# Kernel tuning notes

Hardware: AMD Instinct MI355X
Metric: run time of the kernel (lower is better)

Reference implementation:

```python
import jax, jax.numpy as jnp
import numpy as np

# LSNNParameters defaults (norse)
TAU_SYN_INV = 200.0     # 1/tau_syn
TAU_MEM_INV = 100.0     # 1/tau_mem
TAU_ADAPT_INV = 1.0 / 800.0  # 1/tau_adapt
V_LEAK = 0.0
V_TH = 1.0
V_RESET = 0.0
BETA = 1.8
DT = 0.001

B, IN_F, OUT_F = 8192, 512, 1024


def setup_inputs() -> dict:
    key = jax.random.key(0)
    k0, k1, k2, k3, k4, k5, k6 = jax.random.split(key, 7)
    input_spikes = (jax.random.uniform(k0, (B, IN_F)) < 0.2).astype(jnp.float32)
    z = (jax.random.uniform(k1, (B, OUT_F)) < 0.2).astype(jnp.float32)
    v = jax.random.normal(k2, (B, OUT_F)) * 0.5
    i = jax.random.normal(k3, (B, OUT_F)) * 0.5
    b = jax.random.uniform(k4, (B, OUT_F))
    input_weights = jax.random.normal(k5, (OUT_F, IN_F)) / np.sqrt(IN_F)
    recurrent_weights = jax.random.normal(k6, (OUT_F, OUT_F))
    return {
        "input_spikes": input_spikes,
        "z": z,
        "v": v,
        "i": i,
        "b": b,
        "input_weights": input_weights,
        "recurrent_weights": recurrent_weights,
    }


def reference(input_spikes, z, v, i, b, input_weights, recurrent_weights):
    # One euler step of the LSNN cell (norse lsnn_step).
    # voltage update: dv = dt * tau_mem_inv * ((v_leak - v) + i)
    v_decayed = v + DT * TAU_MEM_INV * ((V_LEAK - v) + i)
    # current decay: di = -dt * tau_syn_inv * i
    i_decayed = i + DT * (-TAU_SYN_INV) * i
    # adaptive threshold relaxes toward v_th
    b_decayed = b + DT * TAU_ADAPT_INV * (V_TH - b)
    # spike condition (heaviside jump)
    z_new = (v_decayed - b_decayed > 0).astype(v.dtype)
    # reset
    v_new = (1.0 - z_new) * v_decayed + z_new * V_RESET
    # current jumps from input + recurrent synapses (x @ W^T, torch linear)
    i_new = (
        i_decayed
        + jnp.einsum("bi,oi->bo", input_spikes, input_weights)
        + jnp.einsum("bo,no->bn", z, recurrent_weights)
    )
    # threshold adaptation
    b_new = b_decayed + z_new * TAU_ADAPT_INV * BETA
    # stack (z, v, i, b) new state -> [4, B, OUT_F]
    return jnp.stack([z_new, v_new, i_new, b_new])
```

## Files before the change

### kernel.cpp

```cpp
#include <hip/hip_runtime.h>

#define B_ROWS 8192
#define IN_F 512
#define OUT_F 1024
#define K_TOT 1536

#define BM 64
#define BN 64
#define BK 64
#define NITER (K_TOT / BK)

#define A4_COUNT (B_ROWS * (K_TOT / 4))
#define W4_COUNT (OUT_F  * (K_TOT / 4))
#define P4_COUNT (B_ROWS * OUT_F / 4)
#define PRE_TASKS (A4_COUNT + W4_COUNT + P4_COUNT)

typedef short bfrag __attribute__((ext_vector_type(8)));
typedef float f4    __attribute__((ext_vector_type(4)));

__device__ __forceinline__ unsigned int pack2bf(float a, float b) {
    unsigned int ua = __float_as_uint(a);
    unsigned int ub = __float_as_uint(b);
    ua = (ua + 0x7fffu + ((ua >> 16) & 1u)) >> 16;
    ub = (ub + 0x7fffu + ((ub >> 16) & 1u)) & 0xffff0000u;
    return ua | ub;
}

__global__ __launch_bounds__(256) void precast_pointwise(
    const float* __restrict__ spikes, const float* __restrict__ zin,
    const float* __restrict__ Wi,     const float* __restrict__ Wr,
    const float* __restrict__ vin,    const float* __restrict__ iin,
    const float* __restrict__ bin,
    unsigned short* __restrict__ Abf, unsigned short* __restrict__ Wbf,
    float* __restrict__ out)
{
    const int idx = blockIdx.x * 256 + threadIdx.x;
    if (idx < A4_COUNT + W4_COUNT) {
        const float* src;
        unsigned short* dst;
        if (idx < A4_COUNT) {
            const int row = idx / 384, c4 = idx - row * 384;
            src = (c4 < 128) ? spikes + (size_t)row * IN_F + c4 * 4
                             : zin    + (size_t)row * OUT_F + (c4 - 128) * 4;
            dst = Abf + (size_t)idx * 4;
        } else {
            const int w = idx - A4_COUNT;
            const int row = w / 384, c4 = w - row * 384;
            src = (c4 < 128) ? Wi + (size_t)row * IN_F + c4 * 4
                             : Wr + (size_t)row * OUT_F + (c4 - 128) * 4;
            dst = Wbf + (size_t)w * 4;
        }
        const float4 v = *(const float4*)src;
        uint2 pk = { pack2bf(v.x, v.y), pack2bf(v.z, v.w) };
        *(uint2*)dst = pk;
    } else {
        const int j = idx - (A4_COUNT + W4_COUNT);
        const size_t PL = (size_t)B_ROWS * OUT_F;
        const float4 v = ((const float4*)vin)[j];
        const float4 i = ((const float4*)iin)[j];
        const float4 b = ((const float4*)bin)[j];
        float4 z, vn, bn;
        {
            const float v_dec = v.x + 0.1f * ((0.0f - v.x) + i.x);
            const float b_dec = b.x + 1.25e-06f * (1.0f - b.x);
            z.x = (v_dec - b_dec > 0.0f) ? 1.0f : 0.0f;
            vn.x = (1.0f - z.x) * v_dec;
            bn.x = b_dec + z.x * 0.00225f;
        }
        {
            const float v_dec = v.y + 0.1f * ((0.0f - v.y) + i.y);
            const float b_dec = b.y + 1.25e-06f * (1.0f - b.y);
            z.y = (v_dec - b_dec > 0.0f) ? 1.0f : 0.0f;
            vn.y = (1.0f - z.y) * v_dec;
            bn.y = b_dec + z.y * 0.00225f;
        }
        {
            const float v_dec = v.z + 0.1f * ((0.0f - v.z) + i.z);
            const float b_dec = b.z + 1.25e-06f * (1.0f - b.z);
            z.z = (v_dec - b_dec > 0.0f) ? 1.0f : 0.0f;
            vn.z = (1.0f - z.z) * v_dec;
            bn.z = b_dec + z.z * 0.00225f;
        }
        {
            const float v_dec = v.w + 0.1f * ((0.0f - v.w) + i.w);
            const float b_dec = b.w + 1.25e-06f * (1.0f - b.w);
            z.w = (v_dec - b_dec > 0.0f) ? 1.0f : 0.0f;
            vn.w = (1.0f - z.w) * v_dec;
            bn.w = b_dec + z.w * 0.00225f;
        }
        ((float4*)out)[j]            = z;
        ((float4*)(out + PL))[j]     = vn;
        ((float4*)(out + 3 * PL))[j] = bn;
    }
}

__global__ __launch_bounds__(256, 4) void lsnn_gemm(
    const unsigned short* __restrict__ Abf,
    const unsigned short* __restrict__ Wbf,
    const float* __restrict__ iin,
    float* __restrict__ out)
{
    __shared__ unsigned short As[2][BM * BK];
    __shared__ unsigned short Ws[2][BN * BK];

    const int tid = threadIdx.x;
    const int bid = blockIdx.x;
    const int n0 = (bid & 15) * BN;
    const int m0 = (bid >> 4) * BM;

    const int lane = tid & 63;
    const int wave = tid >> 6;
    const int wm = (wave >> 1) * 32;
    const int wn = (wave & 1) * 32;
    const int lr = lane & 15;
    const int lq = lane >> 4;

    f4 acc[2][2];
    #pragma unroll
    for (int a = 0; a < 2; ++a)
        #pragma unroll
        for (int b = 0; b < 2; ++b)
            acc[a][b] = (f4)0.0f;

    const unsigned short* Ab = Abf + (size_t)m0 * K_TOT;
    const unsigned short* Wb = Wbf + (size_t)n0 * K_TOT;

    int rr[2], cc_[2], jj[2];
    #pragma unroll
    for (int p = 0; p < 2; ++p) {
        const int q = p * 256 + wave * 64 + lane;
        rr[p] = q >> 3;
        cc_[p] = (q & 7) ^ (rr[p] & 7);
        jj[p] = p * 256 + wave * 64;
    }

    auto stage = [&](int buf, int kt) {
        #pragma unroll
        for (int p = 0; p < 2; ++p)
            __builtin_amdgcn_global_load_lds(
                (const __attribute__((address_space(1))) void*)(Ab + (size_t)rr[p] * K_TOT + kt + cc_[p] * 8),
                (__attribute__((address_space(3))) void*)(&As[buf][jj[p] * 8]),
                16, 0, 0);
        #pragma unroll
        for (int p = 0; p < 2; ++p)
            __builtin_amdgcn_global_load_lds(
                (const __attribute__((address_space(1))) void*)(Wb + (size_t)rr[p] * K_TOT + kt + cc_[p] * 8),
                (__attribute__((address_space(3))) void*)(&Ws[buf][jj[p] * 8]),
                16, 0, 0);
    };

    stage(0, 0);
    __syncthreads();

    int cur = 0;
    for (int it = 0; it < NITER; ++it) {
        if (it + 1 < NITER) stage(cur ^ 1, (it + 1) * BK);

        #pragma unroll
        for (int ks = 0; ks < 2; ++ks) {
            const int cc = ks * 4 + lq;
            bfrag af[2], wf[2];
            #pragma unroll
            for (int t = 0; t < 2; ++t) {
                const int row = wm + t * 16 + lr;
                af[t] = *(const bfrag*)&As[cur][row * BK + ((cc ^ (row & 7)) << 3)];
            }
            #pragma unroll
            for (int t = 0; t < 2; ++t) {
                const int row = wn + t * 16 + lr;
                wf[t] = *(const bfrag*)&Ws[cur][row * BK + ((cc ^ (row & 7)) << 3)];
            }
            #pragma unroll
            for (int tm = 0; tm < 2; ++tm)
                #pragma unroll
                for (int tn = 0; tn < 2; ++tn)
                    acc[tm][tn] = __builtin_amdgcn_mfma_f32_16x16x32_bf16(
                        af[tm], wf[tn], acc[tm][tn], 0, 0, 0);
        }

        __syncthreads();
        cur ^= 1;
    }

    const size_t PL2 = 2 * (size_t)B_ROWS * OUT_F;
    #pragma unroll
    for (int tm = 0; tm < 2; ++tm) {
        #pragma unroll
        for (int tn = 0; tn < 2; ++tn) {
            #pragma unroll
            for (int r = 0; r < 4; ++r) {
                const int gm = m0 + wm + tm * 16 + lq * 4 + r;
                const int gn = n0 + wn + tn * 16 + lr;
                const size_t idx = (size_t)gm * OUT_F + gn;
                const float i = iin[idx];
                out[PL2 + idx] = (i - 0.2f * i) + acc[tm][tn][r];
            }
        }
    }
}

extern "C" void kernel_launch(void* const* d_in, const int* in_sizes, int n_in,
                              void* d_out, int out_size, void* d_ws, size_t ws_size,
                              hipStream_t stream) {
    const float* spikes = (const float*)d_in[0];
    const float* z      = (const float*)d_in[1];
    const float* v      = (const float*)d_in[2];
    const float* i      = (const float*)d_in[3];
    const float* b      = (const float*)d_in[4];
    const float* Wi     = (const float*)d_in[5];
    const float* Wr     = (const float*)d_in[6];
    float* out = (float*)d_out;

    unsigned short* Abf = (unsigned short*)d_ws;
    unsigned short* Wbf = Abf + (size_t)B_ROWS * K_TOT;

    precast_pointwise<<<PRE_TASKS / 256, 256, 0, stream>>>(
        spikes, z, Wi, Wr, v, i, b, Abf, Wbf, out);

    const int grid = (B_ROWS / BM) * (OUT_F / BN);
    lsnn_gemm<<<grid, 256, 0, stream>>>(Abf, Wbf, i, out);
}
```

Measured before the change: 308.5 us.

## Move pointwise state update into GEMM kernel as interleaved blocks

The memory-bound pointwise update of z, v and b moves out of the precast kernel and into the GEMM launch as extra blocks, interleaved in groups of eight with the GEMM tiles. This lets streaming bandwidth work overlap with the matrix-core work instead of running before it. The precast kernel now handles only the bf16 casts, with four float4 loads per thread to increase memory-level parallelism. Output stores use nontemporal hints. The interleaved blocks do uneven amounts of work, which could unbalance scheduling, and the mixed kernel shares register and LDS limits with the GEMM path.

Result: no change. 314.5 us (+1.9%).

```diff
diff --git a/kernel.cpp b/kernel.cpp
--- a/kernel.cpp
+++ b/kernel.cpp
@@ -12,8 +12,10 @@
 
 #define A4_COUNT (B_ROWS * (K_TOT / 4))
 #define W4_COUNT (OUT_F  * (K_TOT / 4))
-#define P4_COUNT (B_ROWS * OUT_F / 4)
-#define PRE_TASKS (A4_COUNT + W4_COUNT + P4_COUNT)
+#define CAST_BLOCKS ((A4_COUNT + W4_COUNT) / 1024)
+#define GEMM_BLOCKS ((B_ROWS / BM) * (OUT_F / BN))
+#define P_BLOCKS ((B_ROWS * OUT_F / 4) / 1024)
+#define FUSED_BLOCKS (GEMM_BLOCKS + P_BLOCKS)
 
 typedef short bfrag __attribute__((ext_vector_type(8)));
 typedef float f4    __attribute__((ext_vector_type(4)));
@@ -26,87 +28,102 @@
     return ua | ub;
 }
 
-__global__ __launch_bounds__(256) void precast_pointwise(
+__global__ __launch_bounds__(256) void precast_aw(
     const float* __restrict__ spikes, const float* __restrict__ zin,
     const float* __restrict__ Wi,     const float* __restrict__ Wr,
-    const float* __restrict__ vin,    const float* __restrict__ iin,
-    const float* __restrict__ bin,
-    unsigned short* __restrict__ Abf, unsigned short* __restrict__ Wbf,
-    float* __restrict__ out)
+    unsigned short* __restrict__ Abf, unsigned short* __restrict__ Wbf)
 {
-    const int idx = blockIdx.x * 256 + threadIdx.x;
-    if (idx < A4_COUNT + W4_COUNT) {
-        const float* src;
-        unsigned short* dst;
+    const int base = blockIdx.x * 1024 + threadIdx.x;
+    const float4* src[4];
+    #pragma unroll
+    for (int k = 0; k < 4; ++k) {
+        const int idx = base + k * 256;
         if (idx < A4_COUNT) {
             const int row = idx / 384, c4 = idx - row * 384;
-            src = (c4 < 128) ? spikes + (size_t)row * IN_F + c4 * 4
-                             : zin    + (size_t)row * OUT_F + (c4 - 128) * 4;
-            dst = Abf + (size_t)idx * 4;
+            src[k] = (const float4*)((c4 < 128)
+                         ? spikes + (size_t)row * IN_F + c4 * 4
+                         : zin    + (size_t)row * OUT_F + (c4 - 128) * 4);
         } else {
             const int w = idx - A4_COUNT;
             const int row = w / 384, c4 = w - row * 384;
-            src = (c4 < 128) ? Wi + (size_t)row * IN_F + c4 * 4
-                             : Wr + (size_t)row * OUT_F + (c4 - 128) * 4;
-            dst = Wbf + (size_t)w * 4;
-        }
-        const float4 v = *(const float4*)src;
-        uint2 pk = { pack2bf(v.x, v.y), pack2bf(v.z, v.w) };
+            src[k] = (const float4*)((c4 < 128)
+                         ? Wi + (size_t)row * IN_F + c4 * 4
+                         : Wr + (size_t)row * OUT_F + (c4 - 128) * 4);
+        }
+    }
+    float4 val[4];
+    #pragma unroll
+    for (int k = 0; k < 4; ++k) val[k] = *src[k];
+    #pragma unroll
+    for (int k = 0; k < 4; ++k) {
+        const int idx = base + k * 256;
+        unsigned short* dst = (idx < A4_COUNT)
+                                  ? Abf + (size_t)idx * 4
+                                  : Wbf + (size_t)(idx - A4_COUNT) * 4;
+        uint2 pk = { pack2bf(val[k].x, val[k].y), pack2bf(val[k].z, val[k].w) };
         *(uint2*)dst = pk;
-    } else {
-        const int j = idx - (A4_COUNT + W4_COUNT);
-        const size_t PL = (size_t)B_ROWS * OUT_F;
-        const float4 v = ((const float4*)vin)[j];
-        const float4 i = ((const float4*)iin)[j];
-        const float4 b = ((const float4*)bin)[j];
-        float4 z, vn, bn;
-        {
-            const float v_dec = v.x + 0.1f * ((0.0f - v.x) + i.x);
-            const float b_dec = b.x + 1.25e-06f * (1.0f - b.x);
-            z.x = (v_dec - b_dec > 0.0f) ? 1.0f : 0.0f;
-            vn.x = (1.0f - z.x) * v_dec;
-            bn.x = b_dec + z.x * 0.00225f;
-        }
-        {
-            const float v_dec = v.y + 0.1f * ((0.0f - v.y) + i.y);
-            const float b_dec = b.y + 1.25e-06f * (1.0f - b.y);
-            z.y = (v_dec - b_dec > 0.0f) ? 1.0f : 0.0f;
-            vn.y = (1.0f - z.y) * v_dec;
-            bn.y = b_dec + z.y * 0.00225f;
-        }
-        {
-            const float v_dec = v.z + 0.1f * ((0.0f - v.z) + i.z);
-            const float b_dec = b.z + 1.25e-06f * (1.0f - b.z);
-            z.z = (v_dec - b_dec > 0.0f) ? 1.0f : 0.0f;
-            vn.z = (1.0f - z.z) * v_dec;
-            bn.z = b_dec + z.z * 0.00225f;
-        }
-        {
-            const float v_dec = v.w + 0.1f * ((0.0f - v.w) + i.w);
-            const float b_dec = b.w + 1.25e-06f * (1.0f - b.w);
-            z.w = (v_dec - b_dec > 0.0f) ? 1.0f : 0.0f;
-            vn.w = (1.0f - z.w) * v_dec;
-            bn.w = b_dec + z.w * 0.00225f;
-        }
-        ((float4*)out)[j]            = z;
-        ((float4*)(out + PL))[j]     = vn;
-        ((float4*)(out + 3 * PL))[j] = bn;
+    }
+}
+
+__device__ __forceinline__ void pointwise_block(
+    int pb, int tid,
+    const float* __restrict__ vin, const float* __restrict__ iin,
+    const float* __restrict__ bin, float* __restrict__ out)
+{
+    const size_t PL = (size_t)B_ROWS * OUT_F;
+    const int base = pb * 1024 + tid;
+    const f4* v4 = (const f4*)vin;
+    const f4* i4 = (const f4*)iin;
+    const f4* b4 = (const f4*)bin;
+    f4 vv[4], ii[4], bb[4];
+    #pragma unroll
+    for (int k = 0; k < 4; ++k) vv[k] = v4[base + k * 256];
+    #pragma unroll
+    for (int k = 0; k < 4; ++k) ii[k] = i4[base + k * 256];
+    #pragma unroll
+    for (int k = 0; k < 4; ++k) bb[k] = b4[base + k * 256];
+    #pragma unroll
+    for (int k = 0; k < 4; ++k) {
+        f4 z, vn, bn;
+        #pragma unroll
+        for (int c = 0; c < 4; ++c) {
+            const float v_dec = vv[k][c] + 0.1f * (ii[k][c] - vv[k][c]);
+            const float b_dec = bb[k][c] + 1.25e-06f * (1.0f - bb[k][c]);
+            const float zz = (v_dec - b_dec > 0.0f) ? 1.0f : 0.0f;
+            z[c]  = zz;
+            vn[c] = (1.0f - zz) * v_dec;
+            bn[c] = b_dec + zz * 0.00225f;
+        }
+        const int j = base + k * 256;
+        __builtin_nontemporal_store(z,  (f4*)out + j);
+        __builtin_nontemporal_store(vn, (f4*)(out + PL) + j);
+        __builtin_nontemporal_store(bn, (f4*)(out + 3 * PL) + j);
     }
 }
 
 __global__ __launch_bounds__(256, 4) void lsnn_gemm(
     const unsigned short* __restrict__ Abf,
     const unsigned short* __restrict__ Wbf,
+    const float* __restrict__ vin,
     const float* __restrict__ iin,
+    const float* __restrict__ bin,
     float* __restrict__ out)
 {
     __shared__ unsigned short As[2][BM * BK];
     __shared__ unsigned short Ws[2][BN * BK];
 
     const int tid = threadIdx.x;
-    const int bid = blockIdx.x;
-    const int n0 = (bid & 15) * BN;
-    const int m0 = (bid >> 4) * BM;
+    const int octet = blockIdx.x >> 3;
+    const int sub   = blockIdx.x & 7;
+    const int id    = (octet >> 1) * 8 + sub;
+
+    if (octet & 1) {
+        pointwise_block(id, tid, vin, iin, bin, out);
+        return;
+    }
+
+    const int n0 = (id & 15) * BN;
+    const int m0 = (id >> 4) * BM;
 
     const int lane = tid & 63;
     const int wave = tid >> 6;
@@ -193,7 +210,8 @@
                 const int gn = n0 + wn + tn * 16 + lr;
                 const size_t idx = (size_t)gm * OUT_F + gn;
                 const float i = iin[idx];
-                out[PL2 + idx] = (i - 0.2f * i) + acc[tm][tn][r];
+                __builtin_nontemporal_store((i - 0.2f * i) + acc[tm][tn][r],
+                                            &out[PL2 + idx]);
             }
         }
     }
@@ -214,9 +232,7 @@
     unsigned short* Abf = (unsigned short*)d_ws;
     unsigned short* Wbf = Abf + (size_t)B_ROWS * K_TOT;
 
-    precast_pointwise<<<PRE_TASKS / 256, 256, 0, stream>>>(
-        spikes, z, Wi, Wr, v, i, b, Abf, Wbf, out);
-
-    const int grid = (B_ROWS / BM) * (OUT_F / BN);
-    lsnn_gemm<<<grid, 256, 0, stream>>>(Abf, Wbf, i, out);
-}
+    precast_aw<<<CAST_BLOCKS, 256, 0, stream>>>(spikes, z, Wi, Wr, Abf, Wbf);
+
+    lsnn_gemm<<<FUSED_BLOCKS, 256, 0, stream>>>(Abf, Wbf, v, i, b, out);
+}
```
